# Kernel optimization log

Hardware: AMD Instinct MI355X
Metric: run time of the kernel (lower is better)

The kernel has to match this reference:

```python
import jax, jax.numpy as jnp
import numpy as np
from jax import lax

H = 100  # hidden size hard-coded in the module


def setup_inputs() -> dict:
    key = jax.random.key(0)
    ks = jax.random.split(key, 13)
    T = 8192
    s = 1.0 / np.sqrt(H)  # torch LSTMCell/Linear init scale
    f32 = jnp.float32
    return {
        "input": jax.random.normal(ks[0], (T, 1), f32),
        "encoder_state_h": jax.random.normal(ks[1], (1, H), f32),
        "encoder_state_c": jax.random.normal(ks[2], (1, H), f32),
        "w_ih1": jax.random.normal(ks[3], (4 * H, 1), f32) * s,
        "w_hh1": jax.random.normal(ks[4], (4 * H, H), f32) * s,
        "b_ih1": jax.random.normal(ks[5], (4 * H,), f32) * s,
        "b_hh1": jax.random.normal(ks[6], (4 * H,), f32) * s,
        "w_ih2": jax.random.normal(ks[7], (4 * H, H), f32) * s,
        "w_hh2": jax.random.normal(ks[8], (4 * H, H), f32) * s,
        "b_ih2": jax.random.normal(ks[9], (4 * H,), f32) * s,
        "b_hh2": jax.random.normal(ks[10], (4 * H,), f32) * s,
        "w_lin": jax.random.normal(ks[11], (1, H), f32) * s,
        "b_lin": jax.random.normal(ks[12], (1,), f32) * s,
        "future": 1024,
    }


def _lstm_cell(x, h, c, w_ih, w_hh, b_ih, b_hh):
    # torch.nn.LSTMCell: gates ordered i, f, g, o
    gates = x @ w_ih.T + h @ w_hh.T + b_ih + b_hh  # (1, 4H)
    i, f, g, o = jnp.split(gates, 4, axis=-1)
    c_new = jax.nn.sigmoid(f) * c + jax.nn.sigmoid(i) * jnp.tanh(g)
    h_new = jax.nn.sigmoid(o) * jnp.tanh(c_new)
    return h_new, c_new


def reference(input, encoder_state_h, encoder_state_c,
              w_ih1, w_hh1, b_ih1, b_hh1,
              w_ih2, w_hh2, b_ih2, b_hh2,
              w_lin, b_lin, future):
    dt = input.dtype

    def step(carry, x_t):
        h1, c1, h2, c2 = carry
        h1, c1 = _lstm_cell(x_t, h1, c1, w_ih1, w_hh1, b_ih1, b_hh1)
        h2, c2 = _lstm_cell(h1, h2, c2, w_ih2, w_hh2, b_ih2, b_hh2)
        y = h2 @ w_lin.T + b_lin  # (1, 1)
        return (h1, c1, h2, c2), y

    carry0 = (encoder_state_h, encoder_state_c,
              jnp.zeros((1, H), dt), jnp.zeros((1, H), dt))
    xs = input[:, None, :]  # (T, 1, 1): per-step (1,1) input as in chunk(dim=0)
    carry, ys = lax.scan(step, carry0, xs)
    seq_out = ys[:, 0, 0][None, :]  # (1, T)

    if future:
        def fstep(carry, _):
            h1, c1, h2, c2, y = carry
            h1, c1 = _lstm_cell(y, h1, c1, w_ih1, w_hh1, b_ih1, b_hh1)
            h2, c2 = _lstm_cell(h1, h2, c2, w_ih2, w_hh2, b_ih2, b_hh2)
            y = h2 @ w_lin.T + b_lin
            return (h1, c1, h2, c2, y), y

        fcarry0 = carry + (ys[-1],)
        _, fys = lax.scan(fstep, fcarry0, None, length=future)
        fut_out = fys[:, 0, 0][None, :]  # (1, future)
        return jnp.concatenate([seq_out, fut_out], axis=1)  # (1, T+future)
    return seq_out
```

## Files before the change

### kernel.cpp

```cpp
#include <hip/hip_runtime.h>
#include <math.h>


#define HH 100
#define NT 256
#define ROWS 400
#define SPIN_CAP 2000000u

#define OFF_APROG  0
#define OFF_P2PROG 128
#define OFF_BPROG  256
#define OFF_YPROG  384
#define OFF_YSLOT  512
#define OFF_RING   16384

__device__ __forceinline__ float rl(float v, int k) {
    return __int_as_float(__builtin_amdgcn_readlane(__float_as_int(v), k));
}
__device__ __forceinline__ unsigned san(unsigned v) { return v > 0x00FFFFFFu ? 0u : v; }
__device__ __forceinline__ void rel(unsigned* p, unsigned v) {
    __hip_atomic_store(p, v, __ATOMIC_RELEASE, __HIP_MEMORY_SCOPE_AGENT);
}
__device__ __forceinline__ float ld_f(const float* p) {
    return __hip_atomic_load((float*)p, __ATOMIC_RELAXED, __HIP_MEMORY_SCOPE_AGENT);
}
__device__ __forceinline__ void st_wt(float* p, float v) {
    __hip_atomic_store(p, v, __ATOMIC_RELAXED, __HIP_MEMORY_SCOPE_AGENT);
}
__device__ __forceinline__ void wait_ge(unsigned* p, unsigned need, unsigned& cache) {
    if (cache >= need) return;
    unsigned s = 0;
    do {
        cache = san(__hip_atomic_load(p, __ATOMIC_RELAXED, __HIP_MEMORY_SCOPE_AGENT));
    } while (cache < need && ++s < SPIN_CAP);
    __builtin_amdgcn_fence(__ATOMIC_ACQUIRE, "agent");
}
__device__ __forceinline__ float fast_sigm(float x) {
    return __builtin_amdgcn_rcpf(1.0f + __expf(-x));
}
__device__ __forceinline__ float fast_tanh(float x) {
    return fmaf(-2.0f, __builtin_amdgcn_rcpf(1.0f + __expf(2.0f * x)), 1.0f);
}

__device__ __forceinline__ void dot2rows(const float* w0, const float* w1,
                                         float hv0, float hv1,
                                         float& accA, float& accB) {
    float a0 = 0.f, a1 = 0.f, b0 = 0.f, b1 = 0.f;
    #pragma unroll
    for (int k = 0; k < 64; k += 2) {
        float h0 = rl(hv0, k), h1 = rl(hv0, k + 1);
        a0 = fmaf(w0[k],     h0, a0);
        a1 = fmaf(w0[k + 1], h1, a1);
        b0 = fmaf(w1[k],     h0, b0);
        b1 = fmaf(w1[k + 1], h1, b1);
    }
    #pragma unroll
    for (int k = 0; k < 36; k += 2) {
        float h0 = rl(hv1, k), h1 = rl(hv1, k + 1);
        a0 = fmaf(w0[64 + k],     h0, a0);
        a1 = fmaf(w0[64 + k + 1], h1, a1);
        b0 = fmaf(w1[64 + k],     h0, b0);
        b1 = fmaf(w1[64 + k + 1], h1, b1);
    }
    accA += (a0 + a1);
    accB += (b0 + b1);
}

extern "C" __global__ void __launch_bounds__(NT, 1)
decoder_kernel(const float* __restrict__ input,
               const float* __restrict__ enc_h,
               const float* __restrict__ enc_c,
               const float* __restrict__ w_ih1,
               const float* __restrict__ w_hh1,
               const float* __restrict__ b_ih1,
               const float* __restrict__ b_hh1,
               const float* __restrict__ w_ih2,
               const float* __restrict__ w_hh2,
               const float* __restrict__ b_ih2,
               const float* __restrict__ b_hh2,
               const float* __restrict__ w_lin,
               const float* __restrict__ b_lin,
               float* __restrict__ out,
               char* __restrict__ ws,
               int T, int F, int S)
{
    const int tid = threadIdx.x;
    const int l = tid & 63;
    const int w = tid >> 6;
    unsigned* a_prog  = (unsigned*)(ws + OFF_APROG);
    unsigned* p2_prog = (unsigned*)(ws + OFF_P2PROG);
    unsigned* b_prog  = (unsigned*)(ws + OFF_BPROG);
    unsigned* y_prog  = (unsigned*)(ws + OFF_YPROG);
    float* y_slot = (float*)(ws + OFF_YSLOT);
    float* ring1  = (float*)(ws + OFF_RING);
    float* ring2  = ring1 + (size_t)S * HH;
    const int smask = S - 1;
    const int TOT = T + F;

    const bool gi_lane = (l < 25);
    const bool go_lane = (l >= 32 && l < 57);
    const int cell = 25 * w + (gi_lane ? l : (go_lane ? (l - 32) : 0));
    const int gj0 = gi_lane ? cell : (go_lane ? cell + 200 : 0);
    const int gj1 = gi_lane ? cell + 100 : (go_lane ? cell + 300 : 0);

    if (blockIdx.x == 0) {
        __shared__ __align__(16) float h1s[2][128];
        float w0[HH], w1[HH];
        const float wx0 = w_ih1[gj0];
        const float wx1 = w_ih1[gj1];
        const float bi0 = b_ih1[gj0] + b_hh1[gj0];
        const float bi1 = b_ih1[gj1] + b_hh1[gj1];
        #pragma unroll
        for (int k = 0; k < HH; ++k) w0[k] = w_hh1[gj0 * HH + k];
        #pragma unroll
        for (int k = 0; k < HH; ++k) w1[k] = w_hh1[gj1 * HH + k];
        float c1 = gi_lane ? enc_c[cell] : 0.f;
        if (tid < 128) { h1s[0][tid] = 0.f; h1s[1][tid] = 0.f; }
        __syncthreads();
        if (tid < HH) h1s[0][tid] = enc_h[tid];
        __syncthreads();

        unsigned cp2 = 0, cy = 0;
        for (int t = 0; t < TOT; ++t) {
            const float* hb = h1s[t & 1];
            float x = 0.f;
            if (t < T) x = input[t];
            float hv0 = hb[l];
            float hv1 = hb[64 + l];
            float accA = bi0, accB = bi1;
            dot2rows(w0, w1, hv0, hv1, accA, accB);
            if (t >= T) {
                wait_ge(y_prog, (unsigned)(t - T + 1), cy);
                x = ld_f(&y_slot[t - T]);
            }
            accA = fmaf(x, wx0, accA);
            accB = fmaf(x, wx1, accB);
            float vA = go_lane ? fast_tanh(accA) : fast_sigm(accA);
            float vB = fast_sigm(accB);
            float gg = __shfl_xor(vA, 32);
            float go = __shfl_xor(vB, 32);
            if (t >= S) wait_ge(p2_prog, (unsigned)(t - S + 1), cp2);
            if (gi_lane) {
                c1 = fmaf(vB, c1, vA * gg);
                float h = go * fast_tanh(c1);
                h1s[(t + 1) & 1][cell] = h;
                st_wt(&ring1[(size_t)(t & smask) * HH + cell], h);
            }
            __syncthreads();
            if (tid == 0) rel(a_prog, (unsigned)(t + 1));
        }
    } else if (blockIdx.x == 1) {
        const bool has2 = tid < (ROWS - NT);
        const int j0 = tid, j1 = has2 ? NT + tid : 0;
        float w0[HH], w1[HH];
        const float bi0 = b_ih2[j0] + b_hh2[j0];
        const float bi1 = b_ih2[j1] + b_hh2[j1];
        #pragma unroll
        for (int k = 0; k < HH; ++k) w0[k] = w_ih2[j0 * HH + k];
        #pragma unroll
        for (int k = 0; k < HH; ++k) w1[k] = w_ih2[j1 * HH + k];

        unsigned ca = 0, cb = 0;
        for (int t = 0; t < TOT; ++t) {
            wait_ge(a_prog, (unsigned)(t + 1), ca);
            const float* rp = ring1 + (size_t)(t & smask) * HH;
            float hv0 = ld_f(rp + l);
            float hv1 = (l < 36) ? ld_f(rp + 64 + l) : 0.f;
            float accA = bi0, accB = bi1;
            dot2rows(w0, w1, hv0, hv1, accA, accB);
            if (t >= S) wait_ge(b_prog, (unsigned)(t - S + 1), cb);
            float* wp = ring2 + (size_t)(t & smask) * ROWS;
            st_wt(&wp[j0], accA);
            if (has2) st_wt(&wp[j1], accB);
            __syncthreads();
            if (tid == 0) rel(p2_prog, (unsigned)(t + 1));
        }
    } else {
        __shared__ __align__(16) float h2s[2][128];
        __shared__ float yp2[2][4];
        float w0[HH], w1[HH];
        #pragma unroll
        for (int k = 0; k < HH; ++k) w0[k] = w_hh2[gj0 * HH + k];
        #pragma unroll
        for (int k = 0; k < HH; ++k) w1[k] = w_hh2[gj1 * HH + k];
        const float wl = gi_lane ? w_lin[cell] : 0.f;
        const float bl = b_lin[0];
        float c2 = 0.f;
        if (tid < 128) { h2s[0][tid] = 0.f; h2s[1][tid] = 0.f; }
        __syncthreads();

        unsigned cp = 0;
        for (int t = 0; t < TOT; ++t) {
            if (tid == 0 && t > 0) {
                const float* yq = yp2[(t - 1) & 1];
                float y = yq[0] + yq[1] + yq[2] + yq[3] + bl;
                if (t - 1 >= T - 1) {
                    st_wt(&y_slot[(t - 1) - (T - 1)], y);
                    rel(y_prog, (unsigned)(t - T + 1));
                }
                rel(b_prog, (unsigned)t);
                out[t - 1] = y;
            }
            const float* hb = h2s[t & 1];
            float hv0 = hb[l];
            float hv1 = hb[64 + l];
            const float* pp = ring2 + (size_t)(t & smask) * ROWS;
            float accA = 0.f, accB = 0.f, preA, preB;
            if (t < T) {
                wait_ge(p2_prog, (unsigned)(t + 1), cp);
                preA = ld_f(pp + gj0);
                preB = ld_f(pp + gj1);
                dot2rows(w0, w1, hv0, hv1, accA, accB);
            } else {
                dot2rows(w0, w1, hv0, hv1, accA, accB);
                wait_ge(p2_prog, (unsigned)(t + 1), cp);
                preA = ld_f(pp + gj0);
                preB = ld_f(pp + gj1);
            }
            accA += preA;
            accB += preB;
            float vA = go_lane ? fast_tanh(accA) : fast_sigm(accA);
            float vB = fast_sigm(accB);
            float gg = __shfl_xor(vA, 32);
            float go = __shfl_xor(vB, 32);
            float py = 0.f;
            if (gi_lane) {
                c2 = fmaf(vB, c2, vA * gg);
                float h = go * fast_tanh(c2);
                h2s[(t + 1) & 1][cell] = h;
                py = h * wl;
            }
            py += __shfl_down(py, 32);
            py += __shfl_down(py, 16);
            py += __shfl_down(py, 8);
            py += __shfl_down(py, 4);
            py += __shfl_down(py, 2);
            py += __shfl_down(py, 1);
            if (l == 0) yp2[t & 1][w] = py;
            __syncthreads();
        }
        if (tid == 0) {
            const float* yq = yp2[(TOT - 1) & 1];
            out[TOT - 1] = yq[0] + yq[1] + yq[2] + yq[3] + bl;
        }
    }
}

extern "C" void kernel_launch(void* const* d_in, const int* in_sizes, int n_in,
                              void* d_out, int out_size, void* d_ws, size_t ws_size,
                              hipStream_t stream) {
    const float* input = (const float*)d_in[0];
    const float* enc_h = (const float*)d_in[1];
    const float* enc_c = (const float*)d_in[2];
    const float* w_ih1 = (const float*)d_in[3];
    const float* w_hh1 = (const float*)d_in[4];
    const float* b_ih1 = (const float*)d_in[5];
    const float* b_hh1 = (const float*)d_in[6];
    const float* w_ih2 = (const float*)d_in[7];
    const float* w_hh2 = (const float*)d_in[8];
    const float* b_ih2 = (const float*)d_in[9];
    const float* b_hh2 = (const float*)d_in[10];
    const float* w_lin = (const float*)d_in[11];
    const float* b_lin = (const float*)d_in[12];
    (void)n_in;

    int T = in_sizes[0];
    int F = out_size - T;
    if (F < 0) F = 0;

    int S = 16;
    while ((size_t)OFF_RING + (size_t)S * 2 * (HH + ROWS) * 4 <= ws_size && S < 8192)
        S <<= 1;

    decoder_kernel<<<dim3(3), dim3(NT), 0, stream>>>(
        input, enc_h, enc_c, w_ih1, w_hh1, b_ih1, b_hh1,
        w_ih2, w_hh2, b_ih2, b_hh2, w_lin, b_lin,
        (float*)d_out, (char*)d_ws, T, F, S);
}
```

Before: 17.65 ms.

## Replace block-level release flags with per-wave progress counters and software pipeline

Each wave now publishes its own progress counter after an explicit vmcnt wait, and consumers poll all four counters and take the minimum. This replaces the __syncthreads plus a release store by one thread. The input-projection block also software-pipelines its loop, prefetching the next h1 vector while computing the current one, and delays its progress publication with vmcnt(2). The aim is to take barrier and release-fence latency off the serial recurrence path between the three blocks. In exchange it relies on hand-written waitcnt ordering instead of acquire/release semantics, which is a memory-ordering correctness risk.

```diff
diff --git a/kernel.cpp b/kernel.cpp
--- a/kernel.cpp
+++ b/kernel.cpp
@@ -7,19 +7,27 @@
 #define ROWS 400
 #define SPIN_CAP 2000000u
 
-#define OFF_APROG  0
-#define OFF_P2PROG 128
+#define OFF_AW     0
+#define OFF_P2W    128
 #define OFF_BPROG  256
 #define OFF_YPROG  384
 #define OFF_YSLOT  512
 #define OFF_RING   16384
 
+#define VMCNT0() asm volatile("s_waitcnt vmcnt(0)" ::: "memory")
+#define VMCNT2() asm volatile("s_waitcnt vmcnt(2)" ::: "memory")
+#define LGKM0()  asm volatile("s_waitcnt lgkmcnt(0)" ::: "memory")
+#define CLOB()   asm volatile("" ::: "memory")
+
 __device__ __forceinline__ float rl(float v, int k) {
     return __int_as_float(__builtin_amdgcn_readlane(__float_as_int(v), k));
 }
 __device__ __forceinline__ unsigned san(unsigned v) { return v > 0x00FFFFFFu ? 0u : v; }
-__device__ __forceinline__ void rel(unsigned* p, unsigned v) {
-    __hip_atomic_store(p, v, __ATOMIC_RELEASE, __HIP_MEMORY_SCOPE_AGENT);
+__device__ __forceinline__ unsigned ldu(const unsigned* p) {
+    return san(__hip_atomic_load((unsigned*)p, __ATOMIC_RELAXED, __HIP_MEMORY_SCOPE_AGENT));
+}
+__device__ __forceinline__ void stu(unsigned* p, unsigned v) {
+    __hip_atomic_store(p, v, __ATOMIC_RELAXED, __HIP_MEMORY_SCOPE_AGENT);
 }
 __device__ __forceinline__ float ld_f(const float* p) {
     return __hip_atomic_load((float*)p, __ATOMIC_RELAXED, __HIP_MEMORY_SCOPE_AGENT);
@@ -30,10 +38,24 @@
 __device__ __forceinline__ void wait_ge(unsigned* p, unsigned need, unsigned& cache) {
     if (cache >= need) return;
     unsigned s = 0;
-    do {
-        cache = san(__hip_atomic_load(p, __ATOMIC_RELAXED, __HIP_MEMORY_SCOPE_AGENT));
-    } while (cache < need && ++s < SPIN_CAP);
-    __builtin_amdgcn_fence(__ATOMIC_ACQUIRE, "agent");
+    do { cache = ldu(p); } while (cache < need && ++s < SPIN_CAP);
+    VMCNT0();
+}
+__device__ __forceinline__ void wait_min4(unsigned* q, unsigned need, unsigned& cache) {
+    if (cache >= need) return;
+    unsigned s = 0;
+    for (;;) {
+        unsigned m0 = ldu(q), m1 = ldu(q + 1), m2 = ldu(q + 2), m3 = ldu(q + 3);
+        unsigned a = m0 < m1 ? m0 : m1, b = m2 < m3 ? m2 : m3;
+        cache = a < b ? a : b;
+        if (cache >= need || ++s > SPIN_CAP) break;
+    }
+    VMCNT0();
+}
+__device__ __forceinline__ void bar() {
+    LGKM0();
+    __builtin_amdgcn_s_barrier();
+    CLOB();
 }
 __device__ __forceinline__ float fast_sigm(float x) {
     return __builtin_amdgcn_rcpf(1.0f + __expf(-x));
@@ -87,10 +109,10 @@
     const int tid = threadIdx.x;
     const int l = tid & 63;
     const int w = tid >> 6;
-    unsigned* a_prog  = (unsigned*)(ws + OFF_APROG);
-    unsigned* p2_prog = (unsigned*)(ws + OFF_P2PROG);
-    unsigned* b_prog  = (unsigned*)(ws + OFF_BPROG);
-    unsigned* y_prog  = (unsigned*)(ws + OFF_YPROG);
+    unsigned* aw     = (unsigned*)(ws + OFF_AW);
+    unsigned* p2w    = (unsigned*)(ws + OFF_P2W);
+    unsigned* b_prog = (unsigned*)(ws + OFF_BPROG);
+    unsigned* y_prog = (unsigned*)(ws + OFF_YPROG);
     float* y_slot = (float*)(ws + OFF_YSLOT);
     float* ring1  = (float*)(ws + OFF_RING);
     float* ring2  = ring1 + (size_t)S * HH;
@@ -114,19 +136,22 @@
         for (int k = 0; k < HH; ++k) w0[k] = w_hh1[gj0 * HH + k];
         #pragma unroll
         for (int k = 0; k < HH; ++k) w1[k] = w_hh1[gj1 * HH + k];
-        float c1 = gi_lane ? enc_c[cell] : 0.f;
-        if (tid < 128) { h1s[0][tid] = 0.f; h1s[1][tid] = 0.f; }
-        __syncthreads();
-        if (tid < HH) h1s[0][tid] = enc_h[tid];
+        float cst = gi_lane ? enc_c[cell] : 0.f;
+        if (tid < 128) {
+            h1s[0][tid] = (tid < HH) ? enc_h[tid] : 0.f;
+            h1s[1][tid] = 0.f;
+        }
         __syncthreads();
 
         unsigned cp2 = 0, cy = 0;
         for (int t = 0; t < TOT; ++t) {
-            const float* hb = h1s[t & 1];
+            VMCNT0();
+            if (l == 0 && t > 0) stu(&aw[w], (unsigned)t);
             float x = 0.f;
             if (t < T) x = input[t];
-            float hv0 = hb[l];
-            float hv1 = hb[64 + l];
+            if (t >= S) wait_min4(p2w, (unsigned)(t - S + 1), cp2);
+            float hv0 = h1s[t & 1][l];
+            float hv1 = h1s[t & 1][64 + l];
             float accA = bi0, accB = bi1;
             dot2rows(w0, w1, hv0, hv1, accA, accB);
             if (t >= T) {
@@ -139,16 +164,16 @@
             float vB = fast_sigm(accB);
             float gg = __shfl_xor(vA, 32);
             float go = __shfl_xor(vB, 32);
-            if (t >= S) wait_ge(p2_prog, (unsigned)(t - S + 1), cp2);
             if (gi_lane) {
-                c1 = fmaf(vB, c1, vA * gg);
-                float h = go * fast_tanh(c1);
+                cst = fmaf(vB, cst, vA * gg);
+                float h = go * fast_tanh(cst);
                 h1s[(t + 1) & 1][cell] = h;
                 st_wt(&ring1[(size_t)(t & smask) * HH + cell], h);
             }
-            __syncthreads();
-            if (tid == 0) rel(a_prog, (unsigned)(t + 1));
-        }
+            bar();
+        }
+        VMCNT0();
+        if (l == 0) stu(&aw[w], (unsigned)TOT);
     } else if (blockIdx.x == 1) {
         const bool has2 = tid < (ROWS - NT);
         const int j0 = tid, j1 = has2 ? NT + tid : 0;
@@ -161,19 +186,49 @@
         for (int k = 0; k < HH; ++k) w1[k] = w_ih2[j1 * HH + k];
 
         unsigned ca = 0, cb = 0;
-        for (int t = 0; t < TOT; ++t) {
-            wait_ge(a_prog, (unsigned)(t + 1), ca);
+        wait_min4(aw, 1u, ca);
+        float cv0 = ld_f(ring1 + l);
+        float cv1 = (l < 36) ? ld_f(ring1 + 64 + l) : 0.f;
+        for (int t = 1; t < T; ++t) {
+            VMCNT2();
+            if (l == 0 && t >= 3) stu(&p2w[w], (unsigned)(t - 2));
+            if (t - 1 >= S) wait_ge(b_prog, (unsigned)(t - S), cb);
+            wait_min4(aw, (unsigned)(t + 1), ca);
             const float* rp = ring1 + (size_t)(t & smask) * HH;
-            float hv0 = ld_f(rp + l);
-            float hv1 = (l < 36) ? ld_f(rp + 64 + l) : 0.f;
+            float nv0 = ld_f(rp + l);
+            float nv1 = (l < 36) ? ld_f(rp + 64 + l) : 0.f;
             float accA = bi0, accB = bi1;
-            dot2rows(w0, w1, hv0, hv1, accA, accB);
+            dot2rows(w0, w1, cv0, cv1, accA, accB);
+            float* wp = ring2 + (size_t)((t - 1) & smask) * ROWS;
+            st_wt(wp + j0, accA);
+            if (has2) st_wt(wp + j1, accB);
+            cv0 = nv0; cv1 = nv1;
+        }
+        VMCNT0();
+        if (l == 0) stu(&p2w[w], (unsigned)(T - 1));
+        {
+            if (T - 1 >= S) wait_ge(b_prog, (unsigned)(T - S), cb);
+            float accA = bi0, accB = bi1;
+            dot2rows(w0, w1, cv0, cv1, accA, accB);
+            float* wp = ring2 + (size_t)((T - 1) & smask) * ROWS;
+            st_wt(wp + j0, accA);
+            if (has2) st_wt(wp + j1, accB);
+        }
+        VMCNT0();
+        if (l == 0) stu(&p2w[w], (unsigned)T);
+        for (int t = T; t < TOT; ++t) {
             if (t >= S) wait_ge(b_prog, (unsigned)(t - S + 1), cb);
+            wait_min4(aw, (unsigned)(t + 1), ca);
+            const float* rp = ring1 + (size_t)(t & smask) * HH;
+            cv0 = ld_f(rp + l);
+            cv1 = (l < 36) ? ld_f(rp + 64 + l) : 0.f;
+            float accA = bi0, accB = bi1;
+            dot2rows(w0, w1, cv0, cv1, accA, accB);
             float* wp = ring2 + (size_t)(t & smask) * ROWS;
-            st_wt(&wp[j0], accA);
-            if (has2) st_wt(&wp[j1], accB);
-            __syncthreads();
-            if (tid == 0) rel(p2_prog, (unsigned)(t + 1));
+            st_wt(wp + j0, accA);
+            if (has2) st_wt(wp + j1, accB);
+            VMCNT0();
+            if (l == 0) stu(&p2w[w], (unsigned)(t + 1));
         }
     } else {
         __shared__ __align__(16) float h2s[2][128];
@@ -189,36 +244,35 @@
         if (tid < 128) { h2s[0][tid] = 0.f; h2s[1][tid] = 0.f; }
         __syncthreads();
 
-        unsigned cp = 0;
-        for (int t = 0; t < TOT; ++t) {
-            if (tid == 0 && t > 0) {
-                const float* yq = yp2[(t - 1) & 1];
+        unsigned cpB = 0;
+        for (int u = 0; u < TOT; ++u) {
+            if (tid == 0 && u > 0) {
+                const float* yq = yp2[(u - 1) & 1];
                 float y = yq[0] + yq[1] + yq[2] + yq[3] + bl;
-                if (t - 1 >= T - 1) {
-                    st_wt(&y_slot[(t - 1) - (T - 1)], y);
-                    rel(y_prog, (unsigned)(t - T + 1));
+                stu(b_prog, (unsigned)u);
+                if (u - 1 >= T - 1) {
+                    st_wt(&y_slot[(u - 1) - (T - 1)], y);
+                    VMCNT0();
+                    stu(y_prog, (unsigned)(u - T + 1));
                 }
-                rel(b_prog, (unsigned)t);
-                out[t - 1] = y;
-            }
-            const float* hb = h2s[t & 1];
-            float hv0 = hb[l];
-            float hv1 = hb[64 + l];
-            const float* pp = ring2 + (size_t)(t & smask) * ROWS;
+                out[u - 1] = y;
+            }
+            float hv0 = h2s[u & 1][l];
+            float hv1 = h2s[u & 1][64 + l];
+            const float* pp = ring2 + (size_t)(u & smask) * ROWS;
             float accA = 0.f, accB = 0.f, preA, preB;
-            if (t < T) {
-                wait_ge(p2_prog, (unsigned)(t + 1), cp);
+            if (u < T) {
+                wait_min4(p2w, (unsigned)(u + 1), cpB);
                 preA = ld_f(pp + gj0);
                 preB = ld_f(pp + gj1);
                 dot2rows(w0, w1, hv0, hv1, accA, accB);
             } else {
                 dot2rows(w0, w1, hv0, hv1, accA, accB);
-                wait_ge(p2_prog, (unsigned)(t + 1), cp);
+                wait_min4(p2w, (unsigned)(u + 1), cpB);
                 preA = ld_f(pp + gj0);
                 preB = ld_f(pp + gj1);
             }
-            accA += preA;
-            accB += preB;
+            accA += preA; accB += preB;
             float vA = go_lane ? fast_tanh(accA) : fast_sigm(accA);
             float vB = fast_sigm(accB);
             float gg = __shfl_xor(vA, 32);
@@ -227,7 +281,7 @@
             if (gi_lane) {
                 c2 = fmaf(vB, c2, vA * gg);
                 float h = go * fast_tanh(c2);
-                h2s[(t + 1) & 1][cell] = h;
+                h2s[(u + 1) & 1][cell] = h;
                 py = h * wl;
             }
             py += __shfl_down(py, 32);
@@ -236,8 +290,8 @@
             py += __shfl_down(py, 4);
             py += __shfl_down(py, 2);
             py += __shfl_down(py, 1);
-            if (l == 0) yp2[t & 1][w] = py;
-            __syncthreads();
+            if (l == 0) yp2[u & 1][w] = py;
+            bar();
         }
         if (tid == 0) {
             const float* yq = yp2[(TOT - 1) & 1];
```

New measurement: 16.70 ms. 5.4% less time.
